# Performance work log

Measured on AMD Instinct MI355X. Metric: run time of the kernel, lower is better.

## Reference

```python
import jax, jax.numpy as jnp
import numpy as np
from jax import lax

B, C, H, W = 2, 256, 64, 64
CI = C // 2           # inter_channels = 128
CH = CI // 2          # key/query channels = 64
EPS = 1e-5


def conv1x1(x, w, b):
    # x: [B,C,H,W], w: [O,C], b: [O]
    return jnp.einsum('oc,bchw->bohw', w, x) + b[None, :, None, None]


def bn(x, g, be, m, v):
    inv = (g / jnp.sqrt(v + EPS))[None, :, None, None]
    return (x - m[None, :, None, None]) * inv + be[None, :, None, None]


def setup_inputs() -> dict:
    key = jax.random.key(0)
    ks = jax.random.split(key, 40)
    r = lambda i, shape, sc=0.05: jax.random.normal(ks[i], shape, dtype=jnp.float32) * sc
    u = lambda i, shape: jax.random.uniform(ks[i], shape, dtype=jnp.float32, minval=0.5, maxval=1.5)
    return {
        'q': jax.random.normal(ks[0], (B, C, H, W), dtype=jnp.float32),
        's': jax.random.normal(ks[1], (B, C, H, W), dtype=jnp.float32),
        'scale': jnp.full((1,), 0.3, dtype=jnp.float32),
        'w_v': r(2, (CI, C)), 'b_v': r(3, (CI,)),
        'w_k1': r(4, (CH, C)), 'b_k1': r(5, (CH,)),
        'w_q1': r(6, (CH, C)), 'b_q1': r(7, (CH,)),
        'w_k2': r(8, (CH, C)), 'b_k2': r(9, (CH,)),
        'w_q2': r(10, (CH, C)), 'b_q2': r(11, (CH,)),
        'w_ts': r(12, (CI, C)), 'b_ts': r(13, (CI,)),
        'g_ts': u(14, (CI,)), 'be_ts': r(15, (CI,)), 'm_ts': r(16, (CI,)), 'v_ts': u(17, (CI,)),
        'w_tq': r(18, (CI, C)), 'b_tq': r(19, (CI,)),
        'g_tq': u(20, (CI,)), 'be_tq': r(21, (CI,)), 'm_tq': r(22, (CI,)), 'v_tq': u(23, (CI,)),
        'w_cat': r(24, (CI, 2 * CI, 3, 3)),
        'g_cat': u(25, (CI,)), 'be_cat': r(26, (CI,)), 'm_cat': r(27, (CI,)), 'v_cat': u(28, (CI,)),
    }


def reference(q, s, scale, w_v, b_v, w_k1, b_k1, w_q1, b_q1, w_k2, b_k2, w_q2, b_q2,
              w_ts, b_ts, g_ts, be_ts, m_ts, v_ts,
              w_tq, b_tq, g_tq, be_tq, m_tq, v_tq,
              w_cat, g_cat, be_cat, m_cat, v_cat):
    b_, _, h, w = q.shape
    n = h * w
    # values: [B, N, CI]
    v_q = conv1x1(q, w_v, b_v).reshape(b_, CI, n).transpose(0, 2, 1)
    v_s = conv1x1(s, w_v, b_v).reshape(b_, CI, n).transpose(0, 2, 1)
    # concatenated keys/queries: [B, CI, N]
    k_x = jnp.concatenate([conv1x1(q, w_k1, b_k1), conv1x1(s, w_k2, b_k2)], axis=1).reshape(b_, CI, n)
    q_x = jnp.concatenate([conv1x1(q, w_q1, b_q1), conv1x1(s, w_q2, b_q2)], axis=1).reshape(b_, CI, n)
    # affinity: [B, N, N]
    A_s = jnp.einsum('bcn,bcm->bnm', k_x, q_x)
    attn_s = jax.nn.softmax(A_s, axis=-1)
    attn_q = jax.nn.softmax(jnp.transpose(A_s, (0, 2, 1)), axis=-1)
    # p_s: [B, N, CI] -> [B, CI, H, W]
    p_s = jnp.einsum('bnm,bmc->bnc', attn_s, v_s).transpose(0, 2, 1).reshape(b_, CI, h, w)
    s_t = bn(conv1x1(s, w_ts, b_ts), g_ts, be_ts, m_ts, v_ts)
    q_t = bn(conv1x1(q, w_tq, b_tq), g_tq, be_tq, m_tq, v_tq)
    E_s = scale[0] * p_s + s_t
    q_s_ = jnp.einsum('bnm,bmc->bnc', attn_q, v_q).transpose(0, 2, 1).reshape(b_, CI, h, w)
    E_q = scale[0] * q_s_ + q_t
    cat = jnp.concatenate([E_q, E_s], axis=1)
    conv = lax.conv_general_dilated(cat, w_cat, (1, 1), 'SAME',
                                    dimension_numbers=('NCHW', 'OIHW', 'NCHW'))
    cpam = jax.nn.relu(bn(conv, g_cat, be_cat, m_cat, v_cat))
    return (cpam, E_q, E_s)
```

## Files before the change

kernel.cpp:

```cpp
#include <hip/hip_runtime.h>
#include <hip/hip_bf16.h>

#define NPIX 4096
#define NCH  256
#define CI   128
#define EPS  1e-5f
#define SOFF 20.0f

typedef unsigned short u16;
typedef __attribute__((ext_vector_type(8))) short short8;
typedef __attribute__((ext_vector_type(4))) float f32x4;

__device__ __forceinline__ float bfu2f(u16 u) {
    union { unsigned int i; float f; } x; x.i = ((unsigned int)u) << 16; return x.f;
}
__device__ __forceinline__ u16 f2bfu(float f) {
    union { float ff; unsigned int i; } x; x.ff = f;
    unsigned int r = x.i + 0x7FFFu + ((x.i >> 16) & 1u);
    return (u16)(r >> 16);
}

__device__ __forceinline__ void gload16(const u16* g, u16* l) {
    __builtin_amdgcn_global_load_lds(
        (const __attribute__((address_space(1))) unsigned int*)g,
        (__attribute__((address_space(3))) unsigned int*)l,
        16, 0, 0);
}

__global__ __launch_bounds__(256) void wprep2_kernel(
    const float* __restrict__ w_v,
    const float* __restrict__ w_k1, const float* __restrict__ w_q1,
    const float* __restrict__ w_k2, const float* __restrict__ w_q2,
    const float* __restrict__ w_ts, const float* __restrict__ w_tq,
    u16* __restrict__ Wbf)
{
    int idx = blockIdx.x * 256 + threadIdx.x;
    int src = idx / 98304;
    int r   = idx - src * 98304;
    int o   = r >> 8, c = r & 255;
    float v;
    if (o < 128)      v = w_v[(size_t)o * 256 + c];
    else if (o < 192) v = (src ? w_k2 : w_k1)[(size_t)(o - 128) * 256 + c];
    else if (o < 256) v = (src ? w_q2 : w_q1)[(size_t)(o - 192) * 256 + c];
    else              v = (src ? w_ts : w_tq)[(size_t)(o - 256) * 256 + c];
    Wbf[idx] = f2bfu(v);
}

__global__ __launch_bounds__(256) void proj2_kernel(
    const float* __restrict__ xq, const float* __restrict__ xs,
    const u16* __restrict__ Wbf,
    const float* __restrict__ b_v,
    const float* __restrict__ b_k1, const float* __restrict__ b_q1,
    const float* __restrict__ b_k2, const float* __restrict__ b_q2,
    const float* __restrict__ b_ts, const float* __restrict__ g_ts,
    const float* __restrict__ be_ts, const float* __restrict__ m_ts,
    const float* __restrict__ v_ts,
    const float* __restrict__ b_tq, const float* __restrict__ g_tq,
    const float* __restrict__ be_tq, const float* __restrict__ m_tq,
    const float* __restrict__ v_tq,
    u16* __restrict__ kT, u16* __restrict__ qT,
    u16* __restrict__ vq, u16* __restrict__ vs,
    u16* __restrict__ tq, u16* __restrict__ ts)
{
    __shared__ u16 Xs[64 * 264];
    __shared__ u16 KQ[64 * 136];

    const int tid  = threadIdx.x;
    const int lane = tid & 63;
    const int wid  = tid >> 6;
    const int l16  = lane & 15;
    const int quad = lane >> 4;

    const int n0  = blockIdx.x * 64;
    const int bz  = blockIdx.z;
    const int b   = bz >> 1, src = bz & 1;

    const float* xg = (src ? xs : xq) + (size_t)b * NCH * NPIX + n0;
    #pragma unroll
    for (int k0 = 0; k0 < 64; k0 += 16) {
        float v[16];
        #pragma unroll
        for (int k = 0; k < 16; ++k) {
            int idx = tid + (k0 + k) * 256;
            int c = idx >> 6, n = idx & 63;
            v[k] = xg[(size_t)c * NPIX + n];
        }
        #pragma unroll
        for (int k = 0; k < 16; ++k) {
            int idx = tid + (k0 + k) * 256;
            int c = idx >> 6, n = idx & 63;
            Xs[n * 264 + c] = f2bfu(v[k]);
        }
    }
    __syncthreads();

    const u16* W = Wbf + (size_t)src * 384 * 256;
    const int o0w = wid * 96;
    const float* bk = src ? b_k2 : b_k1;
    const float* bq = src ? b_q2 : b_q1;
    const float* bt = src ? b_ts : b_tq;

    f32x4 acc[24];
    #pragma unroll
    for (int ot = 0; ot < 6; ++ot) {
        int ob = o0w + ot * 16 + quad * 4;
        const float* bp;
        if (ob < 128)      bp = b_v + ob;
        else if (ob < 192) bp = bk + (ob - 128);
        else if (ob < 256) bp = bq + (ob - 192);
        else               bp = bt + (ob - 256);
        float4 b4 = *(const float4*)bp;
        f32x4 iv = (f32x4){b4.x, b4.y, b4.z, b4.w};
        #pragma unroll
        for (int pt = 0; pt < 4; ++pt) acc[ot * 4 + pt] = iv;
    }

    #pragma unroll
    for (int kc = 0; kc < 8; ++kc) {
        short8 bfr[4];
        #pragma unroll
        for (int pt = 0; pt < 4; ++pt)
            bfr[pt] = *(const short8*)&Xs[(pt * 16 + l16) * 264 + kc * 32 + quad * 8];
        #pragma unroll
        for (int ot = 0; ot < 6; ++ot) {
            short8 a = *(const short8*)&W[(size_t)(o0w + ot * 16 + l16) * 256 + kc * 32 + quad * 8];
            #pragma unroll
            for (int pt = 0; pt < 4; ++pt)
                acc[ot * 4 + pt] = __builtin_amdgcn_mfma_f32_16x16x32_bf16(a, bfr[pt], acc[ot * 4 + pt], 0, 0, 0);
        }
    }

    #pragma unroll
    for (int ot = 0; ot < 6; ++ot) {
        int ob = o0w + ot * 16;
        #pragma unroll
        for (int pt = 0; pt < 4; ++pt) {
            int px = pt * 16 + l16;
            f32x4 v4 = acc[ot * 4 + pt];
            if (ob < 128) {
                u16* dst = src ? vs : vq;
                #pragma unroll
                for (int r = 0; r < 4; ++r)
                    dst[((size_t)b * CI + ob + quad * 4 + r) * NPIX + n0 + px] = f2bfu(v4[r]);
            } else if (ob < 256) {
                int colb = (ob < 192) ? (ob - 128) : (64 + ob - 192);
                #pragma unroll
                for (int r = 0; r < 4; ++r)
                    KQ[px * 136 + colb + quad * 4 + r] = f2bfu(v4[r]);
            } else {
                const float* g  = src ? g_ts  : g_tq;
                const float* be = src ? be_ts : be_tq;
                const float* mm = src ? m_ts  : m_tq;
                const float* vv = src ? v_ts  : v_tq;
                u16* dst = src ? ts : tq;
                #pragma unroll
                for (int r = 0; r < 4; ++r) {
                    int oc = ob - 256 + quad * 4 + r;
                    float inv = g[oc] * rsqrtf(vv[oc] + EPS);
                    dst[((size_t)b * CI + oc) * NPIX + n0 + px] =
                        f2bfu((v4[r] - mm[oc]) * inv + be[oc]);
                }
            }
        }
    }
    __syncthreads();

    const int chb = src ? 64 : 0;
    #pragma unroll
    for (int u = 0; u < 4; ++u) {
        int idx = tid + u * 256;
        int px = idx >> 4, oct = idx & 15;
        uint4 val = *(const uint4*)&KQ[px * 136 + oct * 8];
        if (oct < 8)
            *(uint4*)&kT[((size_t)b * NPIX + n0 + px) * CI + chb + oct * 8] = val;
        else
            *(uint4*)&qT[((size_t)b * NPIX + n0 + px) * CI + chb + (oct - 8) * 8] = val;
    }
}

__global__ __launch_bounds__(256) void wprep_kernel(
    const float* __restrict__ w_cat, u16* __restrict__ wT)
{
    const int co = blockIdx.x;
    const float* srcb = w_cat + (size_t)co * 2304;
    u16* dstb = wT + (size_t)co * 2304;
    for (int t = threadIdx.x; t < 2304; t += 256) {
        int ic = t / 9, tap = t - ic * 9;
        dstb[tap * 256 + ic] = f2bfu(srcb[t]);
    }
}

#define AKS_OFF 0
#define AVT_OFF 16384
#define APS_OFF 32768
#define ASMEM_U16 37376

__global__ __launch_bounds__(256) void attn_kernel(
    const u16* __restrict__ kT, const u16* __restrict__ qT,
    const u16* __restrict__ vq, const u16* __restrict__ vs,
    u16* __restrict__ Opart, float* __restrict__ Lpart, int nseg)
{
    __shared__ __align__(16) u16 smem[ASMEM_U16];
    u16* Ps = smem + APS_OFF;

    const int tid  = threadIdx.x;
    const int lane = tid & 63;
    const int wid  = tid >> 6;
    const int l16  = lane & 15;
    const int quad = lane >> 4;
    const int strip = wid * 16;

    const int nt = blockIdx.x;
    const int n0 = nt * 64;
    const int at = blockIdx.y;
    const int z  = blockIdx.z;
    const int b  = z / nseg;
    const int seg = z - b * nseg;

    const u16* Qg = at ? qT : kT;
    const u16* Kg = at ? kT : qT;
    const u16* Vg = at ? vq : vs;

    short8 af[4];
    {
        const u16* Qb = Qg + ((size_t)b * NPIX + n0 + strip + l16) * CI;
        #pragma unroll
        for (int kc = 0; kc < 4; ++kc)
            af[kc] = *(const short8*)&Qb[kc * 32 + quad * 8];
    }

    f32x4 o[8];
    #pragma unroll
    for (int ct = 0; ct < 8; ++ct) o[ct] = (f32x4){0.f, 0.f, 0.f, 0.f};
    float L[4] = {0.f, 0.f, 0.f, 0.f};

    const u16* KgB = Kg + (size_t)b * NPIX * CI;
    const u16* VgB = Vg + (size_t)b * CI * NPIX;

    const int mt0 = seg * (64 / nseg);
    const int mt1 = mt0 + (64 / nseg);

    #define ISSUE_TILE(buf, m0_)                                              \
    {                                                                         \
        u16* kb_ = smem + AKS_OFF + (buf) * 8192;                             \
        u16* vb_ = smem + AVT_OFF + (buf) * 8192;                             \
        _Pragma("unroll")                                                     \
        for (int k = 0; k < 4; ++k) {                                         \
            int sb  = k * 256 + wid * 64;                                     \
            int idx = sb + lane;                                              \
            int row = idx >> 4, segp = idx & 15;                              \
            int segg = segp ^ (row & 15);                                     \
            gload16(KgB + (size_t)((m0_) + row) * CI + segg * 8, kb_ + sb * 8); \
        }                                                                     \
        _Pragma("unroll")                                                     \
        for (int k = 0; k < 4; ++k) {                                         \
            int sb  = k * 256 + wid * 64;                                     \
            int idx = sb + lane;                                              \
            int c = idx >> 3, sgp = idx & 7;                                  \
            int sgg = sgp ^ (c & 7);                                          \
            gload16(VgB + (size_t)c * NPIX + (m0_) + sgg * 8, vb_ + sb * 8);  \
        }                                                                     \
    }

    int cur = 0;
    ISSUE_TILE(0, mt0 * 64);

    for (int mt = mt0; mt < mt1; ++mt) {
        __syncthreads();
        if (mt + 1 < mt1) ISSUE_TILE(1 - cur, (mt + 1) * 64);

        const u16* Ks = smem + AKS_OFF + cur * 8192;
        const u16* Vt = smem + AVT_OFF + cur * 8192;

        f32x4 sv[4];
        #pragma unroll
        for (int ct = 0; ct < 4; ++ct) {
            f32x4 c = (f32x4){0.f, 0.f, 0.f, 0.f};
            #pragma unroll
            for (int kc = 0; kc < 4; ++kc) {
                int s = kc * 4 + quad;
                short8 bf = *(const short8*)&Ks[(ct * 16 + l16) * 128 + ((s ^ l16) * 8)];
                c = __builtin_amdgcn_mfma_f32_16x16x32_bf16(af[kc], bf, c, 0, 0, 0);
            }
            sv[ct] = c;
        }

        #pragma unroll
        for (int r = 0; r < 4; ++r) {
            float p0 = __expf(sv[0][r] - SOFF);
            float p1 = __expf(sv[1][r] - SOFF);
            float p2 = __expf(sv[2][r] - SOFF);
            float p3 = __expf(sv[3][r] - SOFF);
            float tsum = (p0 + p1) + (p2 + p3);
            tsum += __shfl_xor(tsum, 1);
            tsum += __shfl_xor(tsum, 2);
            tsum += __shfl_xor(tsum, 4);
            tsum += __shfl_xor(tsum, 8);
            L[r] += tsum;
            int prow = strip + quad * 4 + r;
            Ps[prow * 72 + 0 * 16 + l16] = f2bfu(p0);
            Ps[prow * 72 + 1 * 16 + l16] = f2bfu(p1);
            Ps[prow * 72 + 2 * 16 + l16] = f2bfu(p2);
            Ps[prow * 72 + 3 * 16 + l16] = f2bfu(p3);
        }

        short8 ap[2];
        #pragma unroll
        for (int kc = 0; kc < 2; ++kc)
            ap[kc] = *(const short8*)&Ps[(strip + l16) * 72 + kc * 32 + quad * 8];
        #pragma unroll
        for (int ct = 0; ct < 8; ++ct) {
            #pragma unroll
            for (int kc = 0; kc < 2; ++kc) {
                int s = kc * 4 + quad;
                short8 bv = *(const short8*)&Vt[(ct * 16 + l16) * 64 + ((s ^ (l16 & 7)) * 8)];
                o[ct] = __builtin_amdgcn_mfma_f32_16x16x32_bf16(ap[kc], bv, o[ct], 0, 0, 0);
            }
        }
        cur ^= 1;
    }

    const size_t tile = (((size_t)(at * 2 + b) * 64 + nt) * nseg + seg);
    u16* Ob = Opart + tile * 8192;
    #pragma unroll
    for (int r = 0; r < 4; ++r) {
        int row = strip + quad * 4 + r;
        #pragma unroll
        for (int ct = 0; ct < 8; ++ct)
            Ob[row * 128 + ct * 16 + l16] = f2bfu(o[ct][r]);
        if (l16 == 0)
            Lpart[tile * 64 + row] = L[r];
    }
    #undef ISSUE_TILE
}

__global__ __launch_bounds__(256) void attn_combine_kernel(
    const u16* __restrict__ Opart, const float* __restrict__ Lpart,
    const u16* __restrict__ tq, const u16* __restrict__ ts,
    const float* __restrict__ scale_p,
    float* __restrict__ out, u16* __restrict__ Ebf, int nseg)
{
    __shared__ float Of[128 * 68];
    __shared__ float invL[64];

    const int tid = threadIdx.x;
    const int nt = blockIdx.x;
    const int n0 = nt * 64;
    const int at = blockIdx.y;
    const int b  = blockIdx.z;

    const u16* Tg = at ? tq : ts;
    float* outE   = out + (size_t)(at ? 1 : 2) * 1048576;
    const int ch0 = at ? 0 : 128;
    const size_t tbase = ((size_t)(at * 2 + b) * 64 + nt) * nseg;

    if (tid < 64) {
        float Lg = 0.f;
        for (int s = 0; s < nseg; ++s) Lg += Lpart[(tbase + s) * 64 + tid];
        invL[tid] = 1.f / Lg;
    }
    __syncthreads();

    #pragma unroll
    for (int k = 0; k < 4; ++k) {
        int idx = tid + k * 256;
        int row = idx >> 4, oct = idx & 15;
        float m[8] = {0.f, 0.f, 0.f, 0.f, 0.f, 0.f, 0.f, 0.f};
        for (int s = 0; s < nseg; ++s) {
            union { uint4 v; u16 u[8]; } pk;
            pk.v = *(const uint4*)&Opart[(tbase + s) * 8192 + row * 128 + oct * 8];
            #pragma unroll
            for (int j = 0; j < 8; ++j) m[j] += bfu2f(pk.u[j]);
        }
        float w = invL[row];
        #pragma unroll
        for (int j = 0; j < 8; ++j)
            Of[(oct * 8 + j) * 68 + row] = m[j] * w;
    }
    __syncthreads();

    float scale = *scale_p;
    const u16* Tb = Tg + (size_t)b * CI * NPIX + n0;
    float* Ob = outE + (size_t)b * CI * NPIX + n0;
    for (int idx = tid; idx < 128 * 64; idx += 256) {
        int c = idx >> 6, r = idx & 63;
        float v = scale * Of[c * 68 + r] + bfu2f(Tb[(size_t)c * NPIX + r]);
        Ob[(size_t)c * NPIX + r] = v;
        Ebf[((size_t)b * NPIX + n0 + r) * NCH + ch0 + c] = f2bfu(v);
    }
}

#define XT_STR 40

__global__ __launch_bounds__(256) void conv_kernel(
    const u16* __restrict__ Ebf,
    const u16* __restrict__ wT,
    const float* __restrict__ g_cat, const float* __restrict__ be_cat,
    const float* __restrict__ m_cat, const float* __restrict__ v_cat,
    float* __restrict__ out)
{
    __shared__ u16 Xt[3 * 66 * XT_STR];

    const int tid  = threadIdx.x;
    const int lane = tid & 63;
    const int wid  = tid >> 6;
    const int l16  = lane & 15;
    const int quad = lane >> 4;

    const int h    = blockIdx.x;
    const int coff = blockIdx.y * 32;
    const int b    = blockIdx.z;

    const int cot = wid >> 1;
    const int pxt = (wid & 1) * 2;

    f32x4 acc[2];
    #pragma unroll
    for (int j = 0; j < 2; ++j) acc[j] = (f32x4){0.f, 0.f, 0.f, 0.f};

    const u16* Eb = Ebf + (size_t)b * NPIX * NCH;

    uint4 xreg[4];
    #pragma unroll
    for (int k = 0; k < 4; ++k) {
        int u = tid + k * 256;
        uint4 val = make_uint4(0u, 0u, 0u, 0u);
        if (u < 792) {
            int part = u & 3, xe = u >> 2;
            int dh = xe / 66, x = xe - dh * 66;
            int gr = h + dh - 1, gc = x - 1;
            if ((unsigned)gr < 64u && (unsigned)gc < 64u)
                val = *(const uint4*)&Eb[((size_t)gr * 64 + gc) * NCH + part * 8];
        }
        xreg[k] = val;
    }

    for (int icc = 0; icc < 8; ++icc) {
        const int ic0 = icc * 32;
        __syncthreads();
        #pragma unroll
        for (int k = 0; k < 4; ++k) {
            int u = tid + k * 256;
            if (u < 792) {
                int part = u & 3, xe = u >> 2;
                int dh = xe / 66, x = xe - dh * 66;
                *(uint4*)&Xt[(dh * 66 + x) * XT_STR + part * 8] = xreg[k];
            }
        }
        __syncthreads();

        short8 wfrag[9];
        #pragma unroll
        for (int tap = 0; tap < 9; ++tap) {
            int co = coff + cot * 16 + l16;
            wfrag[tap] = *(const short8*)&wT[((size_t)co * 9 + tap) * 256 + ic0 + quad * 8];
        }

        if (icc < 7) {
            #pragma unroll
            for (int k = 0; k < 4; ++k) {
                int u = tid + k * 256;
                uint4 val = make_uint4(0u, 0u, 0u, 0u);
                if (u < 792) {
                    int part = u & 3, xe = u >> 2;
                    int dh = xe / 66, x = xe - dh * 66;
                    int gr = h + dh - 1, gc = x - 1;
                    if ((unsigned)gr < 64u && (unsigned)gc < 64u)
                        val = *(const uint4*)&Eb[((size_t)gr * 64 + gc) * NCH + ic0 + 32 + part * 8];
                }
                xreg[k] = val;
            }
        }

        #pragma unroll
        for (int tap = 0; tap < 9; ++tap) {
            const int dh = tap / 3, dw = tap % 3;
            short8 bf[2];
            #pragma unroll
            for (int j = 0; j < 2; ++j) {
                int x = (pxt + j) * 16 + l16 + dw;
                bf[j] = *(const short8*)&Xt[(dh * 66 + x) * XT_STR + quad * 8];
            }
            #pragma unroll
            for (int j = 0; j < 2; ++j)
                acc[j] = __builtin_amdgcn_mfma_f32_16x16x32_bf16(wfrag[tap], bf[j], acc[j], 0, 0, 0);
        }
    }

    #pragma unroll
    for (int r = 0; r < 4; ++r) {
        int co = coff + cot * 16 + quad * 4 + r;
        float inv = g_cat[co] * rsqrtf(v_cat[co] + EPS);
        float mm  = m_cat[co];
        float be  = be_cat[co];
        #pragma unroll
        for (int j = 0; j < 2; ++j) {
            int wcol = (pxt + j) * 16 + l16;
            float v = (acc[j][r] - mm) * inv + be;
            out[((size_t)b * CI + co) * NPIX + h * 64 + wcol] = fmaxf(v, 0.f);
        }
    }
}

extern "C" void kernel_launch(void* const* d_in, const int* in_sizes, int n_in,
                              void* d_out, int out_size, void* d_ws, size_t ws_size,
                              hipStream_t stream)
{
    const float* q     = (const float*)d_in[0];
    const float* s     = (const float*)d_in[1];
    const float* scale = (const float*)d_in[2];
    const float* w_v   = (const float*)d_in[3];
    const float* b_v   = (const float*)d_in[4];
    const float* w_k1  = (const float*)d_in[5];
    const float* b_k1  = (const float*)d_in[6];
    const float* w_q1  = (const float*)d_in[7];
    const float* b_q1  = (const float*)d_in[8];
    const float* w_k2  = (const float*)d_in[9];
    const float* b_k2  = (const float*)d_in[10];
    const float* w_q2  = (const float*)d_in[11];
    const float* b_q2  = (const float*)d_in[12];
    const float* w_ts  = (const float*)d_in[13];
    const float* b_ts  = (const float*)d_in[14];
    const float* g_ts  = (const float*)d_in[15];
    const float* be_ts = (const float*)d_in[16];
    const float* m_ts  = (const float*)d_in[17];
    const float* v_ts  = (const float*)d_in[18];
    const float* w_tq  = (const float*)d_in[19];
    const float* b_tq  = (const float*)d_in[20];
    const float* g_tq  = (const float*)d_in[21];
    const float* be_tq = (const float*)d_in[22];
    const float* m_tq  = (const float*)d_in[23];
    const float* v_tq  = (const float*)d_in[24];
    const float* w_cat = (const float*)d_in[25];
    const float* g_cat = (const float*)d_in[26];
    const float* be_cat= (const float*)d_in[27];
    const float* m_cat = (const float*)d_in[28];
    const float* v_cat = (const float*)d_in[29];

    float* out = (float*)d_out;
    u16* ws = (u16*)d_ws;
    const size_t SZ = (size_t)2 * CI * NPIX;
    u16* kT  = ws;
    u16* qT  = kT + SZ;
    u16* vq  = qT + SZ;
    u16* vs  = vq + SZ;
    u16* tq  = vs + SZ;
    u16* ts  = tq + SZ;
    u16* Wbf = ts + SZ;
    u16* B   = Wbf + 196608;
    u16* Ebf = B;
    u16* wTc = B + 2097152;
    u16* Opart = wTc + 294912;

    const size_t fixed_u16 = 6 * SZ + 196608 + 2097152 + 294912;
    int nseg = 1;
    {
        size_t need4 = (fixed_u16 + (size_t)4 * 2097152) * 2 + (size_t)4 * 131072;
        size_t need2 = (fixed_u16 + (size_t)2 * 2097152) * 2 + (size_t)2 * 131072;
        if (ws_size >= need4)      nseg = 4;
        else if (ws_size >= need2) nseg = 2;
    }
    float* Lpart = (float*)(Opart + (size_t)nseg * 256 * 8192);

    dim3 blk(256);
    hipLaunchKernelGGL(wprep2_kernel, dim3(768), blk, 0, stream,
                       w_v, w_k1, w_q1, w_k2, w_q2, w_ts, w_tq, Wbf);
    hipLaunchKernelGGL(proj2_kernel, dim3(64, 1, 4), blk, 0, stream,
                       q, s, Wbf, b_v, b_k1, b_q1, b_k2, b_q2,
                       b_ts, g_ts, be_ts, m_ts, v_ts,
                       b_tq, g_tq, be_tq, m_tq, v_tq,
                       kT, qT, vq, vs, tq, ts);
    hipLaunchKernelGGL(wprep_kernel, dim3(128), blk, 0, stream, w_cat, wTc);
    hipLaunchKernelGGL(attn_kernel, dim3(64, 2, 2 * nseg), blk, 0, stream,
                       kT, qT, vq, vs, Opart, Lpart, nseg);
    hipLaunchKernelGGL(attn_combine_kernel, dim3(64, 2, 2), blk, 0, stream,
                       Opart, Lpart, tq, ts, scale, out, Ebf, nseg);
    hipLaunchKernelGGL(conv_kernel, dim3(64, 4, 2), blk, 0, stream,
                       Ebf, wTc, g_cat, be_cat, m_cat, v_cat, out);
}
```

Before: 254.1 us.

## Fuse weight-prep kernels, transpose attention score MFMA, use per-wave conv tiles

Merges the two weight-conversion kernels into one launch to save a kernel dispatch. In the attention kernel, swaps the MFMA operands so each lane holds a full query row of scores. That lets the row sum reduce across quads with two shuffles and write P as packed 4-element stores instead of four scalar stores. The conv kernel drops the block-wide shared input tile, its register prefetch and the __syncthreads; each wave now loads its own 34-wide halo tile with no cross-wave synchronisation, at the cost of redundant loads and no load/compute overlap.

Result: faster. 243.0 us (-4.4%).

```diff
diff --git a/kernel.cpp b/kernel.cpp
--- a/kernel.cpp
+++ b/kernel.cpp
@@ -27,23 +27,35 @@
         16, 0, 0);
 }
 
-__global__ __launch_bounds__(256) void wprep2_kernel(
+__global__ __launch_bounds__(256) void prep_kernel(
     const float* __restrict__ w_v,
     const float* __restrict__ w_k1, const float* __restrict__ w_q1,
     const float* __restrict__ w_k2, const float* __restrict__ w_q2,
     const float* __restrict__ w_ts, const float* __restrict__ w_tq,
-    u16* __restrict__ Wbf)
+    u16* __restrict__ Wbf,
+    const float* __restrict__ w_cat, u16* __restrict__ wT)
 {
-    int idx = blockIdx.x * 256 + threadIdx.x;
-    int src = idx / 98304;
-    int r   = idx - src * 98304;
-    int o   = r >> 8, c = r & 255;
-    float v;
-    if (o < 128)      v = w_v[(size_t)o * 256 + c];
-    else if (o < 192) v = (src ? w_k2 : w_k1)[(size_t)(o - 128) * 256 + c];
-    else if (o < 256) v = (src ? w_q2 : w_q1)[(size_t)(o - 192) * 256 + c];
-    else              v = (src ? w_ts : w_tq)[(size_t)(o - 256) * 256 + c];
-    Wbf[idx] = f2bfu(v);
+    const int bx = blockIdx.x;
+    if (bx < 768) {
+        int idx = bx * 256 + threadIdx.x;
+        int src = idx / 98304;
+        int r   = idx - src * 98304;
+        int o   = r >> 8, c = r & 255;
+        float v;
+        if (o < 128)      v = w_v[(size_t)o * 256 + c];
+        else if (o < 192) v = (src ? w_k2 : w_k1)[(size_t)(o - 128) * 256 + c];
+        else if (o < 256) v = (src ? w_q2 : w_q1)[(size_t)(o - 192) * 256 + c];
+        else              v = (src ? w_ts : w_tq)[(size_t)(o - 256) * 256 + c];
+        Wbf[idx] = f2bfu(v);
+    } else {
+        int co = bx - 768;
+        const float* srcb = w_cat + (size_t)co * 2304;
+        u16* dstb = wT + (size_t)co * 2304;
+        for (int t = threadIdx.x; t < 2304; t += 256) {
+            int ic = t / 9, tap = t - ic * 9;
+            dstb[tap * 256 + ic] = f2bfu(srcb[t]);
+        }
+    }
 }
 
 __global__ __launch_bounds__(256) void proj2_kernel(
@@ -178,18 +190,6 @@
     }
 }
 
-__global__ __launch_bounds__(256) void wprep_kernel(
-    const float* __restrict__ w_cat, u16* __restrict__ wT)
-{
-    const int co = blockIdx.x;
-    const float* srcb = w_cat + (size_t)co * 2304;
-    u16* dstb = wT + (size_t)co * 2304;
-    for (int t = threadIdx.x; t < 2304; t += 256) {
-        int ic = t / 9, tap = t - ic * 9;
-        dstb[tap * 256 + ic] = f2bfu(srcb[t]);
-    }
-}
-
 #define AKS_OFF 0
 #define AVT_OFF 16384
 #define APS_OFF 32768
@@ -221,18 +221,18 @@
     const u16* Kg = at ? kT : qT;
     const u16* Vg = at ? vq : vs;
 
-    short8 af[4];
+    short8 qf[4];
     {
         const u16* Qb = Qg + ((size_t)b * NPIX + n0 + strip + l16) * CI;
         #pragma unroll
         for (int kc = 0; kc < 4; ++kc)
-            af[kc] = *(const short8*)&Qb[kc * 32 + quad * 8];
+            qf[kc] = *(const short8*)&Qb[kc * 32 + quad * 8];
     }
 
     f32x4 o[8];
     #pragma unroll
     for (int ct = 0; ct < 8; ++ct) o[ct] = (f32x4){0.f, 0.f, 0.f, 0.f};
-    float L[4] = {0.f, 0.f, 0.f, 0.f};
+    float L = 0.f;
 
     const u16* KgB = Kg + (size_t)b * NPIX * CI;
     const u16* VgB = Vg + (size_t)b * CI * NPIX;
@@ -274,35 +274,34 @@
 
         f32x4 sv[4];
         #pragma unroll
-        for (int ct = 0; ct < 4; ++ct) {
+        for (int m2 = 0; m2 < 4; ++m2) {
             f32x4 c = (f32x4){0.f, 0.f, 0.f, 0.f};
             #pragma unroll
             for (int kc = 0; kc < 4; ++kc) {
                 int s = kc * 4 + quad;
-                short8 bf = *(const short8*)&Ks[(ct * 16 + l16) * 128 + ((s ^ l16) * 8)];
-                c = __builtin_amdgcn_mfma_f32_16x16x32_bf16(af[kc], bf, c, 0, 0, 0);
+                short8 kf = *(const short8*)&Ks[(m2 * 16 + l16) * 128 + ((s ^ l16) * 8)];
+                c = __builtin_amdgcn_mfma_f32_16x16x32_bf16(kf, qf[kc], c, 0, 0, 0);
             }
-            sv[ct] = c;
-        }
-
-        #pragma unroll
-        for (int r = 0; r < 4; ++r) {
-            float p0 = __expf(sv[0][r] - SOFF);
-            float p1 = __expf(sv[1][r] - SOFF);
-            float p2 = __expf(sv[2][r] - SOFF);
-            float p3 = __expf(sv[3][r] - SOFF);
-            float tsum = (p0 + p1) + (p2 + p3);
-            tsum += __shfl_xor(tsum, 1);
-            tsum += __shfl_xor(tsum, 2);
-            tsum += __shfl_xor(tsum, 4);
-            tsum += __shfl_xor(tsum, 8);
-            L[r] += tsum;
-            int prow = strip + quad * 4 + r;
-            Ps[prow * 72 + 0 * 16 + l16] = f2bfu(p0);
-            Ps[prow * 72 + 1 * 16 + l16] = f2bfu(p1);
-            Ps[prow * 72 + 2 * 16 + l16] = f2bfu(p2);
-            Ps[prow * 72 + 3 * 16 + l16] = f2bfu(p3);
-        }
+            sv[m2] = c;
+        }
+
+        float Lsum = 0.f;
+        u16* myPs = Ps + (strip + l16) * 72;
+        #pragma unroll
+        for (int m2 = 0; m2 < 4; ++m2) {
+            float p0 = __expf(sv[m2][0] - SOFF);
+            float p1 = __expf(sv[m2][1] - SOFF);
+            float p2 = __expf(sv[m2][2] - SOFF);
+            float p3 = __expf(sv[m2][3] - SOFF);
+            Lsum += (p0 + p1) + (p2 + p3);
+            ushort4 pk;
+            pk.x = f2bfu(p0); pk.y = f2bfu(p1);
+            pk.z = f2bfu(p2); pk.w = f2bfu(p3);
+            *(ushort4*)&myPs[m2 * 16 + quad * 4] = pk;
+        }
+        Lsum += __shfl_xor(Lsum, 16);
+        Lsum += __shfl_xor(Lsum, 32);
+        L += Lsum;
 
         short8 ap[2];
         #pragma unroll
@@ -328,9 +327,9 @@
         #pragma unroll
         for (int ct = 0; ct < 8; ++ct)
             Ob[row * 128 + ct * 16 + l16] = f2bfu(o[ct][r]);
-        if (l16 == 0)
-            Lpart[tile * 64 + row] = L[r];
-    }
+    }
+    if (quad == 0)
+        Lpart[tile * 64 + strip + l16] = L;
     #undef ISSUE_TILE
 }
 
@@ -390,7 +389,7 @@
     }
 }
 
-#define XT_STR 40
+#define CXT_STR 40
 
 __global__ __launch_bounds__(256) void conv_kernel(
     const u16* __restrict__ Ebf,
@@ -399,7 +398,7 @@
     const float* __restrict__ m_cat, const float* __restrict__ v_cat,
     float* __restrict__ out)
 {
-    __shared__ u16 Xt[3 * 66 * XT_STR];
+    __shared__ u16 XtW[4][3 * 34 * CXT_STR];
 
     const int tid  = threadIdx.x;
     const int lane = tid & 63;
@@ -413,63 +412,32 @@
 
     const int cot = wid >> 1;
     const int pxt = (wid & 1) * 2;
+    const int gc0 = pxt * 16 - 1;
 
     f32x4 acc[2];
     #pragma unroll
     for (int j = 0; j < 2; ++j) acc[j] = (f32x4){0.f, 0.f, 0.f, 0.f};
 
     const u16* Eb = Ebf + (size_t)b * NPIX * NCH;
-
-    uint4 xreg[4];
-    #pragma unroll
-    for (int k = 0; k < 4; ++k) {
-        int u = tid + k * 256;
-        uint4 val = make_uint4(0u, 0u, 0u, 0u);
-        if (u < 792) {
-            int part = u & 3, xe = u >> 2;
-            int dh = xe / 66, x = xe - dh * 66;
-            int gr = h + dh - 1, gc = x - 1;
-            if ((unsigned)gr < 64u && (unsigned)gc < 64u)
-                val = *(const uint4*)&Eb[((size_t)gr * 64 + gc) * NCH + part * 8];
-        }
-        xreg[k] = val;
-    }
+    u16* Xw = &XtW[wid][0];
+    const int cobase = coff + cot * 16 + l16;
 
     for (int icc = 0; icc < 8; ++icc) {
         const int ic0 = icc * 32;
-        __syncthreads();
-        #pragma unroll
-        for (int k = 0; k < 4; ++k) {
-            int u = tid + k * 256;
-            if (u < 792) {
-                int part = u & 3, xe = u >> 2;
-                int dh = xe / 66, x = xe - dh * 66;
-                *(uint4*)&Xt[(dh * 66 + x) * XT_STR + part * 8] = xreg[k];
-            }
-        }
-        __syncthreads();
 
         short8 wfrag[9];
         #pragma unroll
-        for (int tap = 0; tap < 9; ++tap) {
-            int co = coff + cot * 16 + l16;
-            wfrag[tap] = *(const short8*)&wT[((size_t)co * 9 + tap) * 256 + ic0 + quad * 8];
-        }
-
-        if (icc < 7) {
-            #pragma unroll
-            for (int k = 0; k < 4; ++k) {
-                int u = tid + k * 256;
-                uint4 val = make_uint4(0u, 0u, 0u, 0u);
-                if (u < 792) {
-                    int part = u & 3, xe = u >> 2;
-                    int dh = xe / 66, x = xe - dh * 66;
-                    int gr = h + dh - 1, gc = x - 1;
-                    if ((unsigned)gr < 64u && (unsigned)gc < 64u)
-                        val = *(const uint4*)&Eb[((size_t)gr * 64 + gc) * NCH + ic0 + 32 + part * 8];
-                }
-                xreg[k] = val;
-            }
+        for (int tap = 0; tap < 9; ++tap)
+            wfrag[tap] = *(const short8*)&wT[((size_t)cobase * 9 + tap) * 256 + ic0 + quad * 8];
+
+        for (int u = lane; u < 408; u += 64) {
+            int part = u & 3, xe = u >> 2;
+            int dh = xe / 34, x = xe - dh * 34;
+            int gr = h + dh - 1, gc = gc0 + x;
+            uint4 val = make_uint4(0u, 0u, 0u, 0u);
+            if ((unsigned)gr < 64u && (unsigned)gc < 64u)
+                val = *(const uint4*)&Eb[((size_t)gr * 64 + gc) * NCH + ic0 + part * 8];
+            *(uint4*)&Xw[(dh * 34 + x) * CXT_STR + part * 8] = val;
         }
 
         #pragma unroll
@@ -478,8 +446,8 @@
             short8 bf[2];
             #pragma unroll
             for (int j = 0; j < 2; ++j) {
-                int x = (pxt + j) * 16 + l16 + dw;
-                bf[j] = *(const short8*)&Xt[(dh * 66 + x) * XT_STR + quad * 8];
+                int x = j * 16 + l16 + dw;
+                bf[j] = *(const short8*)&Xw[(dh * 34 + x) * CXT_STR + quad * 8];
             }
             #pragma unroll
             for (int j = 0; j < 2; ++j)
@@ -563,14 +531,13 @@
     float* Lpart = (float*)(Opart + (size_t)nseg * 256 * 8192);
 
     dim3 blk(256);
-    hipLaunchKernelGGL(wprep2_kernel, dim3(768), blk, 0, stream,
-                       w_v, w_k1, w_q1, w_k2, w_q2, w_ts, w_tq, Wbf);
+    hipLaunchKernelGGL(prep_kernel, dim3(896), blk, 0, stream,
+                       w_v, w_k1, w_q1, w_k2, w_q2, w_ts, w_tq, Wbf, w_cat, wTc);
     hipLaunchKernelGGL(proj2_kernel, dim3(64, 1, 4), blk, 0, stream,
                        q, s, Wbf, b_v, b_k1, b_q1, b_k2, b_q2,
                        b_ts, g_ts, be_ts, m_ts, v_ts,
                        b_tq, g_tq, be_tq, m_tq, v_tq,
                        kT, qT, vq, vs, tq, ts);
-    hipLaunchKernelGGL(wprep_kernel, dim3(128), blk, 0, stream, w_cat, wTc);
     hipLaunchKernelGGL(attn_kernel, dim3(64, 2, 2 * nseg), blk, 0, stream,
                        kT, qT, vq, vs, Opart, Lpart, nseg);
     hipLaunchKernelGGL(attn_combine_kernel, dim3(64, 2, 2), blk, 0, stream,
```
